# Optimization experiments

Measured on AMD Instinct MI355X. Metric: run time of the kernel, lower is better.

The kernel has to match this reference:

```python
import jax, jax.numpy as jnp
import numpy as np

QMAX = 127.0          # int8 clip bound (symmetric, preserve-zero)
QDIV = 127.5          # AQT int8 scale divisor: 2**(bits-1) - 0.5


def _safe(s):
    # avoid div-by-zero for all-zero rows/cols
    return jnp.where(s == 0.0, 1.0, s)


def setup_inputs() -> dict:
    key = jax.random.key(0)
    k1, k2 = jax.random.split(key)
    lhs = jax.random.normal(k1, (8192, 4096), dtype=jnp.float32)
    rhs = jax.random.normal(k2, (4096, 4096), dtype=jnp.float32)
    return {"lhs": lhs, "rhs": rhs}


def reference(lhs, rhs):
    # --- dynamic symmetric int8 quantization (AQT abs-max calibration) ---
    # lhs: contract over axis 1 -> per-row scale [M, 1]
    s_l = _safe(jnp.max(jnp.abs(lhs), axis=1, keepdims=True) / QDIV)
    # rhs: contract over axis 0 -> per-column scale [1, N]
    s_r = _safe(jnp.max(jnp.abs(rhs), axis=0, keepdims=True) / QDIV)

    q_l = jnp.clip(jnp.round(lhs / s_l), -QMAX, QMAX).astype(jnp.int8)
    q_r = jnp.clip(jnp.round(rhs / s_r), -QMAX, QMAX).astype(jnp.int8)

    # --- integer matmul with int32 accumulation ---
    acc = jax.lax.dot_general(
        q_l, q_r,
        dimension_numbers=(((1,), (0,)), ((), ())),
        preferred_element_type=jnp.int32,
    )

    # --- dequantize: outer product of per-row / per-column scales ---
    return acc.astype(jnp.float32) * s_l * s_r
```

## Files before the change

kernel.cpp:

```cpp
#include <hip/hip_runtime.h>
#include <stdint.h>

#define M_DIM 8192
#define N_DIM 4096
#define K_DIM 4096
#define QMAXF 127.0f
#define QDIVF 127.5f

typedef int v4i __attribute__((ext_vector_type(4)));

typedef __attribute__((address_space(3))) void lds_void_t;
typedef __attribute__((address_space(1))) const void glb_void_t;

static __device__ __forceinline__ void load_lds16(const void* g, void* l) {
    __builtin_amdgcn_global_load_lds((glb_void_t*)g, (lds_void_t*)l, 16, 0, 0);
}

__global__ __launch_bounds__(256) void row_quant_kernel(
        const float* __restrict__ lhs, float* __restrict__ sL,
        int8_t* __restrict__ ql) {
    const int row = blockIdx.x;
    const float4* rp = (const float4*)(lhs + (size_t)row * K_DIM);
    const int t = threadIdx.x;
    float4 v[4];
    float m = 0.0f;
#pragma unroll
    for (int i = 0; i < 4; ++i) {
        v[i] = rp[t + i * 256];
        m = fmaxf(m, fmaxf(fmaxf(fabsf(v[i].x), fabsf(v[i].y)),
                           fmaxf(fabsf(v[i].z), fabsf(v[i].w))));
    }
#pragma unroll
    for (int off = 32; off; off >>= 1) m = fmaxf(m, __shfl_down(m, off, 64));
    __shared__ float wmax[4];
    if ((t & 63) == 0) wmax[t >> 6] = m;
    __syncthreads();
    const float mm = fmaxf(fmaxf(wmax[0], wmax[1]), fmaxf(wmax[2], wmax[3]));
    float s = mm / QDIVF;
    s = (s == 0.0f) ? 1.0f : s;
    if (t == 0) sL[row] = s;
    unsigned* qo = (unsigned*)ql + (size_t)row * 1024;
#pragma unroll
    for (int i = 0; i < 4; ++i) {
        int q0 = (int)fminf(fmaxf(rintf(v[i].x / s), -QMAXF), QMAXF);
        int q1 = (int)fminf(fmaxf(rintf(v[i].y / s), -QMAXF), QMAXF);
        int q2 = (int)fminf(fmaxf(rintf(v[i].z / s), -QMAXF), QMAXF);
        int q3 = (int)fminf(fmaxf(rintf(v[i].w / s), -QMAXF), QMAXF);
        qo[t + i * 256] = (q0 & 255) | ((q1 & 255) << 8) | ((q2 & 255) << 16)
                        | ((unsigned)(q3 & 255) << 24);
    }
}

__global__ __launch_bounds__(256) void col_absmax_kernel(
        const float* __restrict__ rhs, unsigned* __restrict__ bits) {
    const int col = blockIdx.x * 256 + threadIdx.x;
    const int r0 = blockIdx.y * 64;
    float m = 0.0f;
#pragma unroll 4
    for (int r = 0; r < 64; ++r)
        m = fmaxf(m, fabsf(rhs[(size_t)(r0 + r) * N_DIM + col]));
    atomicMax(&bits[col], __float_as_uint(m));
}

__global__ __launch_bounds__(256) void col_scale_kernel(
        const unsigned* __restrict__ bits, float* __restrict__ sR) {
    const int c = blockIdx.x * 256 + threadIdx.x;
    float s = __uint_as_float(bits[c]) / QDIVF;
    sR[c] = (s == 0.0f) ? 1.0f : s;
}

__global__ __launch_bounds__(256) void quant_rhs_t_kernel(
        const float* __restrict__ rhs, const float* __restrict__ sR,
        int8_t* __restrict__ qbT) {
    __shared__ __align__(16) int8_t lt[64][80];
    const int n0 = blockIdx.x * 64;
    const int k0 = blockIdx.y * 64;
    const int t = threadIdx.x;
    const int nloc = t & 63;
    const int kq = (t >> 6) * 16;
    const float s = sR[n0 + nloc];
#pragma unroll
    for (int i = 0; i < 4; ++i) {
        unsigned pack = 0;
#pragma unroll
        for (int j = 0; j < 4; ++j) {
            int kk = kq + i * 4 + j;
            float x = rhs[(size_t)(k0 + kk) * N_DIM + n0 + nloc];
            int q = (int)fminf(fmaxf(rintf(x / s), -QMAXF), QMAXF);
            pack |= (unsigned)(q & 255) << (8 * j);
        }
        *(unsigned*)&lt[nloc][kq + i * 4] = pack;
    }
    __syncthreads();
    const int nn = t >> 2, ch = t & 3;
    v4i val = *(const v4i*)&lt[nn][ch * 16];
    *(v4i*)&qbT[(size_t)(n0 + nn) * K_DIM + k0 + ch * 16] = val;
}


#define BAR() do { asm volatile("" ::: "memory");          \
                   __builtin_amdgcn_s_barrier();           \
                   asm volatile("" ::: "memory"); } while (0)

#define VMCNT(N) asm volatile("s_waitcnt vmcnt(%0)" :: "n"(N) : "memory")

#define STAGE_A(h, kt, bq) \
    load_lds16(gA0 + (size_t)((h) * 128) * K_DIM + (size_t)(kt) * 64, \
               lds + (bq) * 16384 + (h) * 8192 + sdst)
#define STAGE_B(h, kt, bq) \
    load_lds16(gB0 + (size_t)((h) * 128) * K_DIM + (size_t)(kt) * 64, \
               lds + 65536 + (bq) * 16384 + (h) * 8192 + sdst)

#define MFMA16(NB)                                                              \
    _Pragma("unroll") for (int mm = 0; mm < 4; ++mm)                            \
    _Pragma("unroll") for (int nn = 0; nn < 4; ++nn)                            \
        acc[mm][(NB) + nn] = __builtin_amdgcn_mfma_i32_16x16x64_i8(             \
            af[mm], bf[nn], acc[mm][(NB) + nn], 0, 0, 0);

#define TILE(KT, BUF, S, VM) do {                                               \
                        \
    _Pragma("unroll") for (int mm = 0; mm < 4; ++mm)                            \
        af[mm] = *(const v4i*)(lds + (BUF) * 16384 + aoff[mm]);                 \
    _Pragma("unroll") for (int nn = 0; nn < 4; ++nn)                            \
        bf[nn] = *(const v4i*)(lds + (BUF) * 16384 + boff[nn]);                 \
    if (S) { STAGE_A(0, (KT) + 3, ((BUF) + 3) & 3);                             \
             STAGE_A(1, (KT) + 3, ((BUF) + 3) & 3); }                           \
    BAR();                                                                      \
    __builtin_amdgcn_s_setprio(1); MFMA16(0); __builtin_amdgcn_s_setprio(0);    \
    BAR();                                                                      \
                 \
    _Pragma("unroll") for (int nn = 0; nn < 4; ++nn)                            \
        bf[nn] = *(const v4i*)(lds + (BUF) * 16384 + boff[4 + nn]);             \
    if (S) { STAGE_B(0, (KT) + 3, ((BUF) + 3) & 3);                             \
             STAGE_B(1, (KT) + 3, ((BUF) + 3) & 3); }                           \
    VMCNT(VM);                                                                  \
    BAR();                                                                      \
    __builtin_amdgcn_s_setprio(1); MFMA16(4); __builtin_amdgcn_s_setprio(0);    \
    BAR();                                                                      \
} while (0)

__global__ __launch_bounds__(512, 2) void gemm_i8_kernel(
        const int8_t* __restrict__ qa, const int8_t* __restrict__ qbT,
        const float* __restrict__ sL, const float* __restrict__ sR,
        float* __restrict__ out) {
    __shared__ __align__(16) int8_t lds[131072];

    const int t = threadIdx.x;
    const int wave = t >> 6;
    const int lane = t & 63;

    const int bid = blockIdx.x;
    const int swz = (bid & 7) * 64 + (bid >> 3);
    const int brow = (swz & 31) * 256;
    const int bcol = (swz >> 5) * 256;

    const int wm = (wave >> 1) * 64;
    const int wn = (wave & 1) * 128;

    int aoff[4], boff[8];
#pragma unroll
    for (int m = 0; m < 4; ++m) {
        int row = wm + m * 16 + (lane & 15);
        aoff[m] = row * 64 + (((lane >> 4) ^ ((row >> 1) & 3)) * 16);
    }
#pragma unroll
    for (int n = 0; n < 8; ++n) {
        int row = wn + n * 16 + (lane & 15);
        boff[n] = 65536 + row * 64 + (((lane >> 4) ^ ((row >> 1) & 3)) * 16);
    }

    v4i acc[4][8];
#pragma unroll
    for (int m = 0; m < 4; ++m)
#pragma unroll
        for (int n = 0; n < 8; ++n) acc[m][n] = (v4i){0, 0, 0, 0};

    const int srow = t >> 2;
    const int lc = (t & 3) ^ ((srow >> 1) & 3);
    const int8_t* gA0 = qa  + (size_t)(brow + srow) * K_DIM + lc * 16;
    const int8_t* gB0 = qbT + (size_t)(bcol + srow) * K_DIM + lc * 16;
    const int sdst = t * 16;

    v4i af[4], bf[4];

    STAGE_A(0, 0, 0); STAGE_A(1, 0, 0); STAGE_B(0, 0, 0); STAGE_B(1, 0, 0);
    STAGE_A(0, 1, 1); STAGE_A(1, 1, 1); STAGE_B(0, 1, 1); STAGE_B(1, 1, 1);
    STAGE_A(0, 2, 2); STAGE_A(1, 2, 2); STAGE_B(0, 2, 2); STAGE_B(1, 2, 2);
    VMCNT(8);
    BAR();

    for (int kt = 0; kt < 60; kt += 4) {
        TILE(kt + 0, 0, 1, 8);
        TILE(kt + 1, 1, 1, 8);
        TILE(kt + 2, 2, 1, 8);
        TILE(kt + 3, 3, 1, 8);
    }
    TILE(60, 0, 1, 8);
    TILE(61, 1, 0, 4);
    TILE(62, 2, 0, 0);
    TILE(63, 3, 0, 0);

    const int r4 = (lane >> 4) * 4;
    const int cc = lane & 15;
#pragma unroll
    for (int m = 0; m < 4; ++m) {
        const int grow0 = brow + wm + m * 16 + r4;
        const float s0 = sL[grow0 + 0];
        const float s1 = sL[grow0 + 1];
        const float s2 = sL[grow0 + 2];
        const float s3 = sL[grow0 + 3];
#pragma unroll
        for (int n = 0; n < 8; ++n) {
            const int gcol = bcol + wn + n * 16 + cc;
            const float sc = sR[gcol];
            float* o = out + (size_t)grow0 * N_DIM + gcol;
            o[0 * N_DIM] = (float)acc[m][n][0] * s0 * sc;
            o[1 * N_DIM] = (float)acc[m][n][1] * s1 * sc;
            o[2 * N_DIM] = (float)acc[m][n][2] * s2 * sc;
            o[3 * N_DIM] = (float)acc[m][n][3] * s3 * sc;
        }
    }
}

extern "C" void kernel_launch(void* const* d_in, const int* in_sizes, int n_in,
                              void* d_out, int out_size, void* d_ws, size_t ws_size,
                              hipStream_t stream) {
    const float* lhs = (const float*)d_in[0];
    const float* rhs = (const float*)d_in[1];
    float* out = (float*)d_out;

    uint8_t* ws = (uint8_t*)d_ws;
    int8_t* ql    = (int8_t*)ws;
    int8_t* qbT   = (int8_t*)(ws + 33554432);
    float* sL     = (float*)(ws + 50331648);
    float* sR     = (float*)(ws + 50331648 + 32768);
    unsigned* bits = (unsigned*)(ws + 50331648 + 32768 + 16384);

    hipMemsetAsync(bits, 0, N_DIM * sizeof(unsigned), stream);

    row_quant_kernel<<<M_DIM, 256, 0, stream>>>(lhs, sL, ql);
    col_absmax_kernel<<<dim3(N_DIM / 256, K_DIM / 64), 256, 0, stream>>>(rhs, bits);
    col_scale_kernel<<<N_DIM / 256, 256, 0, stream>>>(bits, sR);
    quant_rhs_t_kernel<<<dim3(N_DIM / 64, K_DIM / 64), 256, 0, stream>>>(rhs, sR, qbT);
    gemm_i8_kernel<<<dim3(M_DIM / 256 * N_DIM / 256), 512, 0, stream>>>(ql, qbT, sL, sR, out);
}
```

Before: 223.6 us.

## Software-pipeline LDS fragment reads across k-tiles and cut barriers per tile

Restructures the int8 GEMM main loop so the next k-tile's A and first-half B fragments are read from LDS into a double-buffered register set while the current tile's MFMAs are still issuing. All four global-to-LDS stage loads for tile k+3 are now issued together, and each tile uses one barrier instead of four. The vmcnt waits are retuned to match. This is meant to hide LDS read latency and barrier stalls behind MFMA work, at the cost of more vector registers, which may hurt occupancy at 2 blocks per CU. It also relies on the single barrier being enough to keep the 4-buffer ring free of LDS races.

```diff
diff --git a/kernel.cpp b/kernel.cpp
--- a/kernel.cpp
+++ b/kernel.cpp
@@ -111,31 +111,35 @@
     load_lds16(gB0 + (size_t)((h) * 128) * K_DIM + (size_t)(kt) * 64, \
                lds + 65536 + (bq) * 16384 + (h) * 8192 + sdst)
 
-#define MFMA16(NB)                                                              \
+#define RD_A(BUF, MM) (*(const v4i*)(lds + (BUF) * 16384 + aoff[MM]))
+#define RD_B(BUF, NN) (*(const v4i*)(lds + (BUF) * 16384 + boff[NN]))
+
+#define TILE(KT, BUF, P, S, VM, RDN) do {                                       \
+    _Pragma("unroll") for (int nn = 0; nn < 4; ++nn)                            \
+        bfII[nn] = RD_B(BUF, 4 + nn);                                           \
+    if (S) { STAGE_A(0, (KT) + 3, ((BUF) + 3) & 3);                             \
+             STAGE_A(1, (KT) + 3, ((BUF) + 3) & 3);                             \
+             STAGE_B(0, (KT) + 3, ((BUF) + 3) & 3);                             \
+             STAGE_B(1, (KT) + 3, ((BUF) + 3) & 3); }                           \
+    __builtin_amdgcn_s_setprio(1);                                              \
     _Pragma("unroll") for (int mm = 0; mm < 4; ++mm)                            \
     _Pragma("unroll") for (int nn = 0; nn < 4; ++nn)                            \
-        acc[mm][(NB) + nn] = __builtin_amdgcn_mfma_i32_16x16x64_i8(             \
-            af[mm], bf[nn], acc[mm][(NB) + nn], 0, 0, 0);
-
-#define TILE(KT, BUF, S, VM) do {                                               \
-                        \
+        acc[mm][nn] = __builtin_amdgcn_mfma_i32_16x16x64_i8(                    \
+            af[P][mm], bfI[P][nn], acc[mm][nn], 0, 0, 0);                       \
+    __builtin_amdgcn_s_setprio(0);                                              \
+    if (RDN) {                                                                  \
+        _Pragma("unroll") for (int mm = 0; mm < 4; ++mm)                        \
+            af[(P) ^ 1][mm] = RD_A(((BUF) + 1) & 3, mm);                        \
+        _Pragma("unroll") for (int nn = 0; nn < 4; ++nn)                        \
+            bfI[(P) ^ 1][nn] = RD_B(((BUF) + 1) & 3, nn);                       \
+    }                                                                           \
+    __builtin_amdgcn_s_setprio(1);                                              \
     _Pragma("unroll") for (int mm = 0; mm < 4; ++mm)                            \
-        af[mm] = *(const v4i*)(lds + (BUF) * 16384 + aoff[mm]);                 \
     _Pragma("unroll") for (int nn = 0; nn < 4; ++nn)                            \
-        bf[nn] = *(const v4i*)(lds + (BUF) * 16384 + boff[nn]);                 \
-    if (S) { STAGE_A(0, (KT) + 3, ((BUF) + 3) & 3);                             \
-             STAGE_A(1, (KT) + 3, ((BUF) + 3) & 3); }                           \
-    BAR();                                                                      \
-    __builtin_amdgcn_s_setprio(1); MFMA16(0); __builtin_amdgcn_s_setprio(0);    \
-    BAR();                                                                      \
-                 \
-    _Pragma("unroll") for (int nn = 0; nn < 4; ++nn)                            \
-        bf[nn] = *(const v4i*)(lds + (BUF) * 16384 + boff[4 + nn]);             \
-    if (S) { STAGE_B(0, (KT) + 3, ((BUF) + 3) & 3);                             \
-             STAGE_B(1, (KT) + 3, ((BUF) + 3) & 3); }                           \
+        acc[mm][4 + nn] = __builtin_amdgcn_mfma_i32_16x16x64_i8(                \
+            af[P][mm], bfII[nn], acc[mm][4 + nn], 0, 0, 0);                     \
+    __builtin_amdgcn_s_setprio(0);                                              \
     VMCNT(VM);                                                                  \
-    BAR();                                                                      \
-    __builtin_amdgcn_s_setprio(1); MFMA16(4); __builtin_amdgcn_s_setprio(0);    \
     BAR();                                                                      \
 } while (0)
 
@@ -181,24 +185,28 @@
     const int8_t* gB0 = qbT + (size_t)(bcol + srow) * K_DIM + lc * 16;
     const int sdst = t * 16;
 
-    v4i af[4], bf[4];
+    v4i af[2][4], bfI[2][4], bfII[4];
 
     STAGE_A(0, 0, 0); STAGE_A(1, 0, 0); STAGE_B(0, 0, 0); STAGE_B(1, 0, 0);
     STAGE_A(0, 1, 1); STAGE_A(1, 1, 1); STAGE_B(0, 1, 1); STAGE_B(1, 1, 1);
     STAGE_A(0, 2, 2); STAGE_A(1, 2, 2); STAGE_B(0, 2, 2); STAGE_B(1, 2, 2);
-    VMCNT(8);
+    VMCNT(4);
     BAR();
+#pragma unroll
+    for (int mm = 0; mm < 4; ++mm) af[0][mm] = RD_A(0, mm);
+#pragma unroll
+    for (int nn = 0; nn < 4; ++nn) bfI[0][nn] = RD_B(0, nn);
 
     for (int kt = 0; kt < 60; kt += 4) {
-        TILE(kt + 0, 0, 1, 8);
-        TILE(kt + 1, 1, 1, 8);
-        TILE(kt + 2, 2, 1, 8);
-        TILE(kt + 3, 3, 1, 8);
-    }
-    TILE(60, 0, 1, 8);
-    TILE(61, 1, 0, 4);
-    TILE(62, 2, 0, 0);
-    TILE(63, 3, 0, 0);
+        TILE(kt + 0, 0, 0, 1, 4, 1);
+        TILE(kt + 1, 1, 1, 1, 4, 1);
+        TILE(kt + 2, 2, 0, 1, 4, 1);
+        TILE(kt + 3, 3, 1, 1, 4, 1);
+    }
+    TILE(60, 0, 0, 1, 4, 1);
+    TILE(61, 1, 1, 0, 0, 1);
+    TILE(62, 2, 0, 0, 0, 1);
+    TILE(63, 3, 1, 0, 0, 0);
 
     const int r4 = (lane >> 4) * 4;
     const int cc = lane & 15;
```

After: 220.2 us. No clear change (-1.5%).
